# Kernel tuning notes

Hardware: AMD Instinct MI355X
Metric: run time of the kernel (lower is better)

The kernel has to match this reference:

```python
import jax, jax.numpy as jnp
import numpy as np

NUM_HEADS = 8

def setup_inputs() -> dict:
    key = jax.random.key(0)
    ks = jax.random.split(key, 6)
    B, nW, F_W, ED = 8, 64, 128, 512
    x = jax.random.normal(ks[0], (B * nW, F_W, ED), dtype=jnp.float32)
    adj_mask = jax.random.normal(ks[1], (B, NUM_HEADS, F_W, F_W), dtype=jnp.float32)
    qkv_w = jax.random.normal(ks[2], (ED, 3 * ED), dtype=jnp.float32) * (ED ** -0.5)
    qkv_b = jax.random.normal(ks[3], (3 * ED,), dtype=jnp.float32) * 0.02
    proj_w = jax.random.normal(ks[4], (ED, ED), dtype=jnp.float32) * (ED ** -0.5)
    proj_b = jax.random.normal(ks[5], (ED,), dtype=jnp.float32) * 0.02
    return {"x": x, "adj_mask": adj_mask, "qkv_w": qkv_w, "qkv_b": qkv_b,
            "proj_w": proj_w, "proj_b": proj_b, "B": B, "nW": nW}

def reference(x, adj_mask, qkv_w, qkv_b, proj_w, proj_b, B, nW):
    B_nW, F_W, ED = x.shape
    H = NUM_HEADS
    hd = ED // H
    scale = hd ** -0.5
    # qkv projection: [B_nW, F_W, 3, H, hd]
    qkv = (x @ qkv_w + qkv_b).reshape(B_nW, F_W, 3, H, hd)
    qkv = jnp.transpose(qkv, (2, 0, 3, 1, 4))  # [3, B_nW, H, F_W, hd]
    q, k, v = qkv[0], qkv[1], qkv[2]
    attn = jnp.einsum('bhqd,bhkd->bhqk', q * scale, k)  # [B_nW, H, F_W, F_W]
    # additive adjacency mask, broadcast over windows
    attn = attn.reshape(B, nW, H, F_W, F_W) + adj_mask[:, None]
    attn = attn.reshape(B_nW, H, F_W, F_W)
    attn = jax.nn.softmax(attn, axis=-1)
    out = jnp.einsum('bhqk,bhkd->bhqd', attn, v)  # [B_nW, H, F_W, hd]
    out = jnp.transpose(out, (0, 2, 1, 3)).reshape(B_nW, F_W, ED)
    return out @ proj_w + proj_b
```

## Files before the change

kernel.cpp:

```cpp
#include <hip/hip_runtime.h>

typedef __bf16 bf16_t;
typedef __bf16 bf16x8 __attribute__((ext_vector_type(8)));
typedef float f32x4 __attribute__((ext_vector_type(4)));

#define MFMA16(a, b, c) __builtin_amdgcn_mfma_f32_16x16x32_bf16(a, b, c, 0, 0, 0)

#define F_W 128
#define ED 512
#define NH 8
#define HD 64
#define B_NW 512
#define NTOK 65536

typedef const __attribute__((address_space(1))) void gvoid_t;
typedef __attribute__((address_space(3))) void lvoid_t;
__device__ __forceinline__ void gload16(const void* g, void* l) {
    __builtin_amdgcn_global_load_lds((gvoid_t*)g, (lvoid_t*)l, 16, 0, 0);
}

__device__ __forceinline__ int swz32(int row) { return ((row >> 1) & 3) << 3; }

__global__ __launch_bounds__(256) void prep_kernel(
    const float* __restrict__ qkv_w,
    const float* __restrict__ proj_w,
    bf16_t* __restrict__ qkv_wt,
    bf16_t* __restrict__ proj_wt) {
    int idx = blockIdx.x * 256 + threadIdx.x;
    if (idx < 1536 * 512) {
        int n = idx >> 9, k = idx & 511;
        qkv_wt[idx] = (bf16_t)qkv_w[k * 1536 + n];
    }
    if (idx < 512 * 512) {
        int n = idx >> 9, k = idx & 511;
        proj_wt[idx] = (bf16_t)proj_w[k * 512 + n];
    }
}

__global__ __launch_bounds__(256) void prep_x_kernel(
    const float* __restrict__ x, bf16_t* __restrict__ xbf) {
    size_t i = ((size_t)blockIdx.x * 256 + threadIdx.x) * 8;
    float4 v0 = *(const float4*)(x + i);
    float4 v1 = *(const float4*)(x + i + 4);
    bf16x8 o = {(bf16_t)v0.x, (bf16_t)v0.y, (bf16_t)v0.z, (bf16_t)v0.w,
                (bf16_t)v1.x, (bf16_t)v1.y, (bf16_t)v1.z, (bf16_t)v1.w};
    *(bf16x8*)(xbf + i) = o;
}

__global__ __launch_bounds__(256, 4) void qkv_gemm_kernel(
    const bf16_t* __restrict__ xbf,
    const bf16_t* __restrict__ qkv_wt,
    const float* __restrict__ qkv_b,
    bf16_t* qk_ws,
    bf16_t* vt_ws) {
    __shared__ __align__(16) char sm[18432];
    bf16_t* x_s = (bf16_t*)sm;
    bf16_t* w_s = (bf16_t*)(sm + 8192);
    bf16_t* tb  = (bf16_t*)sm;

    const int tid = threadIdx.x;
    const int wave = tid >> 6, lane = tid & 63;
    const int lrow = lane & 15, lgrp = lane >> 4;
    const int wm = wave >> 1, wn = wave & 1;
    const int bid = blockIdx.x;
    const int idx = bid >> 3;
    const int mt_l = idx / 12;
    const int nt = idx - mt_l * 12;
    const int mtile = (bid & 7) * 64 + mt_l;
    const size_t m0 = (size_t)mtile * 128;
    const int n0 = nt * 128;

    const int row16 = lane >> 2;
    const int scol = ((lane & 3) * 8) ^ swz32(row16);

    f32x4 acc[4][4];
#pragma unroll
    for (int mf = 0; mf < 4; ++mf)
#pragma unroll
        for (int nf = 0; nf < 4; ++nf) acc[mf][nf] = (f32x4)0.0f;

    for (int kc = 0; kc < 16; ++kc) {
        const int k0 = kc * 32;
        __syncthreads();
#pragma unroll
        for (int i = 0; i < 2; ++i) {
            int c = wave * 2 + i;
            gload16(xbf + (m0 + c * 16 + row16) * 512 + k0 + scol, x_s + c * 512);
        }
#pragma unroll
        for (int i = 0; i < 2; ++i) {
            int c = wave * 2 + i;
            gload16(qkv_wt + (size_t)(n0 + c * 16 + row16) * 512 + k0 + scol,
                    w_s + c * 512);
        }
        __syncthreads();

        bf16x8 a[4], b[4];
#pragma unroll
        for (int mf = 0; mf < 4; ++mf) {
            int row = wm * 64 + mf * 16 + lrow;
            a[mf] = *(const bf16x8*)(x_s + row * 32 + ((lgrp * 8) ^ swz32(row)));
        }
#pragma unroll
        for (int nf = 0; nf < 4; ++nf) {
            int rw = wn * 64 + nf * 16 + lrow;
            b[nf] = *(const bf16x8*)(w_s + rw * 32 + ((lgrp * 8) ^ swz32(rw)));
        }
#pragma unroll
        for (int mf = 0; mf < 4; ++mf)
#pragma unroll
            for (int nf = 0; nf < 4; ++nf)
                acc[mf][nf] = MFMA16(a[mf], b[nf], acc[mf][nf]);
    }

    if (nt < 8) {
        const float scale = (nt < 4) ? 0.125f : 1.0f;
#pragma unroll
        for (int nf = 0; nf < 4; ++nf) {
            int col = n0 + wn * 64 + nf * 16 + lrow;
            float bv = qkv_b[col];
#pragma unroll
            for (int mf = 0; mf < 4; ++mf)
#pragma unroll
                for (int j = 0; j < 4; ++j) {
                    int r = wm * 64 + mf * 16 + lgrp * 4 + j;
                    qk_ws[(m0 + r) * 1024 + col] =
                        (bf16_t)((acc[mf][nf][j] + bv) * scale);
                }
        }
    } else {
#pragma unroll
        for (int hh = 0; hh < 2; ++hh) {
            int h = (nt - 8) * 2 + hh;
            __syncthreads();
            if (wn == hh) {
#pragma unroll
                for (int nf = 0; nf < 4; ++nf) {
                    int d = nf * 16 + lrow;
                    float bv = qkv_b[n0 + hh * 64 + d];
#pragma unroll
                    for (int mf = 0; mf < 4; ++mf)
#pragma unroll
                        for (int j = 0; j < 4; ++j) {
                            int r = wm * 64 + mf * 16 + lgrp * 4 + j;
                            tb[r * 72 + d] = (bf16_t)(acc[mf][nf][j] + bv);
                        }
                }
            }
            __syncthreads();
            {
                int d = tid & 63;
                int kh = tid >> 6;
                bf16_t* outp = vt_ws + ((size_t)(mtile * 8 + h) * 64 + d) * 128 + kh * 32;
#pragma unroll
                for (int o = 0; o < 4; ++o) {
                    bf16x8 v;
#pragma unroll
                    for (int e = 0; e < 8; ++e)
                        v[e] = tb[(kh * 32 + o * 8 + e) * 72 + d];
                    *(bf16x8*)(outp + o * 8) = v;
                }
            }
        }
    }
}

__global__ __launch_bounds__(512, 4) void attn_kernel(
    bf16_t* qk_ws,
    const bf16_t* __restrict__ vt_ws,
    const float* __restrict__ adj) {
    __shared__ __align__(16) char sm[32768];
    bf16_t* k_lds  = (bf16_t*)sm;
    bf16_t* vt_lds = (bf16_t*)(sm + 16384);
    bf16_t* pbuf   = (bf16_t*)sm;

    const int tid = threadIdx.x;
    const int wave = tid >> 6, lane = tid & 63;
    const int lrow = lane & 15, lgrp = lane >> 4;
    const int bid = blockIdx.x;
    const int w = (bid & 7) * 64 + (bid >> 6);
    const int h = (bid >> 3) & 7;
    const int bidx = bid & 7;

    bf16_t* qrow = qk_ws + (size_t)w * 128 * 1024;

    {
        const int krow_l = lane >> 3;
        const int kcol_l = ((lane & 7) * 8) ^ ((krow_l & 7) << 3);
#pragma unroll
        for (int i = 0; i < 2; ++i) {
            int c = wave * 2 + i;
            gload16(qrow + (size_t)(c * 8 + krow_l) * 1024 + 512 + h * 64 + kcol_l,
                    k_lds + c * 512);
        }
    }
    {
        const bf16_t* vtb = vt_ws + (size_t)(w * 8 + h) * 64 * 128;
        const int vrow_l = lane >> 4;
#pragma unroll
        for (int i = 0; i < 2; ++i) {
            int c = wave * 2 + i;
            int d = c * 4 + vrow_l;
            int vcol = ((lane & 15) * 8) ^ ((d & 7) << 3);
            gload16(vtb + (size_t)d * 128 + vcol, vt_lds + c * 512);
        }
    }
    bf16x8 aq[2];
    {
        int row = wave * 16 + lrow;
#pragma unroll
        for (int kb = 0; kb < 2; ++kb)
            aq[kb] = *(const bf16x8*)(qrow + (size_t)row * 1024 + h * 64 + kb * 32 + lgrp * 8);
    }
    __syncthreads();

    f32x4 sacc[8];
#pragma unroll
    for (int nf = 0; nf < 8; ++nf) sacc[nf] = (f32x4)0.0f;
#pragma unroll
    for (int kb = 0; kb < 2; ++kb) {
        bf16x8 b[8];
#pragma unroll
        for (int nf = 0; nf < 8; ++nf) {
            int row = nf * 16 + lrow;
            b[nf] = *(const bf16x8*)(k_lds + row * 64 + ((kb * 32 + lgrp * 8) ^ ((row & 7) << 3)));
        }
#pragma unroll
        for (int nf = 0; nf < 8; ++nf)
            sacc[nf] = MFMA16(aq[kb], b[nf], sacc[nf]);
    }

    const float* mbase = adj + ((size_t)(bidx * NH + h)) * F_W * F_W;
#pragma unroll
    for (int j = 0; j < 4; ++j) {
        int row = wave * 16 + lgrp * 4 + j;
        const float* mrow = mbase + (size_t)row * F_W;
        float mx = -1e30f;
#pragma unroll
        for (int nf = 0; nf < 8; ++nf) {
            sacc[nf][j] += mrow[nf * 16 + lrow];
            mx = fmaxf(mx, sacc[nf][j]);
        }
#pragma unroll
        for (int d = 1; d < 16; d <<= 1) mx = fmaxf(mx, __shfl_xor(mx, d));
        float sum = 0.f;
#pragma unroll
        for (int nf = 0; nf < 8; ++nf) {
            float p = exp2f((sacc[nf][j] - mx) * 1.44269504f);
            sacc[nf][j] = p;
            sum += p;
        }
#pragma unroll
        for (int d = 1; d < 16; d <<= 1) sum += __shfl_xor(sum, d);
        float r = 1.0f / sum;
#pragma unroll
        for (int nf = 0; nf < 8; ++nf) sacc[nf][j] *= r;
    }
    __syncthreads();

    f32x4 oacc[4];
#pragma unroll
    for (int nf = 0; nf < 4; ++nf) oacc[nf] = (f32x4)0.0f;

#pragma unroll
    for (int kb = 0; kb < 4; ++kb) {
#pragma unroll
        for (int nn = 0; nn < 2; ++nn) {
            int nf = kb * 2 + nn;
            int kk = nn * 16 + lrow;
#pragma unroll
            for (int j = 0; j < 4; ++j) {
                int r = wave * 16 + lgrp * 4 + j;
                pbuf[r * 40 + kk] = (bf16_t)(sacc[nf][j]);
            }
        }
        __syncthreads();
        bf16x8 a = *(const bf16x8*)(pbuf + (wave * 16 + lrow) * 40 + lgrp * 8);
        bf16x8 b[4];
#pragma unroll
        for (int nf = 0; nf < 4; ++nf) {
            int d = nf * 16 + lrow;
            b[nf] = *(const bf16x8*)(vt_lds + d * 128 + ((kb * 32 + lgrp * 8) ^ ((d & 7) << 3)));
        }
#pragma unroll
        for (int nf = 0; nf < 4; ++nf)
            oacc[nf] = MFMA16(a, b[nf], oacc[nf]);
        __syncthreads();
    }

#pragma unroll
    for (int nf = 0; nf < 4; ++nf) {
        int ocol = h * 64 + nf * 16 + lrow;
#pragma unroll
        for (int j = 0; j < 4; ++j) {
            int r = wave * 16 + lgrp * 4 + j;
            qrow[(size_t)r * 1024 + ocol] = (bf16_t)oacc[nf][j];
        }
    }
}

__global__ __launch_bounds__(256, 4) void proj_kernel(
    const bf16_t* __restrict__ a_g,
    const bf16_t* __restrict__ bt_g,
    const float* __restrict__ bias,
    float* __restrict__ out) {
    __shared__ __align__(16) bf16_t sm_[8192];
    bf16_t* a_s = sm_;
    bf16_t* b_s = sm_ + 4096;
    const int tid = threadIdx.x;
    const int wave = tid >> 6, lane = tid & 63;
    const int lrow = lane & 15, lgrp = lane >> 4;
    const int wm = wave >> 1, wn = wave & 1;
    const int bid = blockIdx.x;
    const int mtile = (bid & 7) * 64 + (bid >> 5);
    const int ntile = (bid >> 3) & 3;
    const size_t m0 = (size_t)mtile * 128;
    const int n0 = ntile * 128;
    const int row16 = lane >> 2;
    const int scol = ((lane & 3) * 8) ^ swz32(row16);

    f32x4 acc[4][4];
#pragma unroll
    for (int mf = 0; mf < 4; ++mf)
#pragma unroll
        for (int nf = 0; nf < 4; ++nf) acc[mf][nf] = (f32x4)0.0f;

    for (int kc = 0; kc < 16; ++kc) {
        const int k0 = kc * 32;
        __syncthreads();
#pragma unroll
        for (int i = 0; i < 2; ++i) {
            int c = wave * 2 + i;
            gload16(a_g + (m0 + c * 16 + row16) * 1024 + k0 + scol, a_s + c * 512);
            gload16(bt_g + (size_t)(n0 + c * 16 + row16) * 512 + k0 + scol, b_s + c * 512);
        }
        __syncthreads();
        bf16x8 a[4], b[4];
#pragma unroll
        for (int mf = 0; mf < 4; ++mf) {
            int row = wm * 64 + mf * 16 + lrow;
            a[mf] = *(const bf16x8*)(a_s + row * 32 + ((lgrp * 8) ^ swz32(row)));
        }
#pragma unroll
        for (int nf = 0; nf < 4; ++nf) {
            int rw = wn * 64 + nf * 16 + lrow;
            b[nf] = *(const bf16x8*)(b_s + rw * 32 + ((lgrp * 8) ^ swz32(rw)));
        }
#pragma unroll
        for (int mf = 0; mf < 4; ++mf)
#pragma unroll
            for (int nf = 0; nf < 4; ++nf)
                acc[mf][nf] = MFMA16(a[mf], b[nf], acc[mf][nf]);
    }

#pragma unroll
    for (int nf = 0; nf < 4; ++nf) {
        int col = n0 + wn * 64 + nf * 16 + lrow;
        float bv = bias[col];
#pragma unroll
        for (int mf = 0; mf < 4; ++mf)
#pragma unroll
            for (int j = 0; j < 4; ++j) {
                size_t row = m0 + wm * 64 + mf * 16 + lgrp * 4 + j;
                out[row * 512 + col] = acc[mf][nf][j] + bv;
            }
    }
}

extern "C" void kernel_launch(void* const* d_in, const int* in_sizes, int n_in,
                              void* d_out, int out_size, void* d_ws, size_t ws_size,
                              hipStream_t stream) {
    const float* x      = (const float*)d_in[0];
    const float* adj    = (const float*)d_in[1];
    const float* qkv_w  = (const float*)d_in[2];
    const float* qkv_b  = (const float*)d_in[3];
    const float* proj_w = (const float*)d_in[4];
    const float* proj_b = (const float*)d_in[5];
    float* out = (float*)d_out;

    bf16_t* qk_ws   = (bf16_t*)d_ws;
    bf16_t* vt_ws   = qk_ws + (size_t)NTOK * 1024;
    bf16_t* qkv_wt  = vt_ws + (size_t)4096 * 64 * 128;
    bf16_t* proj_wt = qkv_wt + 1536 * 512;
    bf16_t* xbf = (bf16_t*)d_out;

    prep_kernel<<<3072, 256, 0, stream>>>(qkv_w, proj_w, qkv_wt, proj_wt);
    prep_x_kernel<<<NTOK * ED / 8 / 256, 256, 0, stream>>>(x, xbf);
    qkv_gemm_kernel<<<6144, 256, 0, stream>>>(xbf, qkv_wt, qkv_b, qk_ws, vt_ws);
    attn_kernel<<<4096, 512, 0, stream>>>(qk_ws, vt_ws, adj);
    proj_kernel<<<2048, 256, 0, stream>>>(qk_ws, proj_wt, proj_b, out);
}
```

Before: 317.2 us.

## Double-buffer activation tiles and load weight fragments directly from global in GEMMs

Both the QKV and projection GEMMs now double-buffer the activation tile in LDS with a 64-wide K step, prefetching the next chunk while computing the current one. This halves the number of barriers per tile. Weight fragments are read straight from global memory (L2-cached) into registers instead of being staged through LDS. The aim is to hide global-load latency and cut synchronisation, at the cost of larger LDS use (32KB) and more registers, which may reduce occupancy under launch_bounds(256,4).

```diff
diff --git a/kernel.cpp b/kernel.cpp
--- a/kernel.cpp
+++ b/kernel.cpp
@@ -53,10 +53,8 @@
     const float* __restrict__ qkv_b,
     bf16_t* qk_ws,
     bf16_t* vt_ws) {
-    __shared__ __align__(16) char sm[18432];
-    bf16_t* x_s = (bf16_t*)sm;
-    bf16_t* w_s = (bf16_t*)(sm + 8192);
-    bf16_t* tb  = (bf16_t*)sm;
+    __shared__ __align__(16) char sm[32768];
+    bf16_t* tb = (bf16_t*)sm;
 
     const int tid = threadIdx.x;
     const int wave = tid >> 6, lane = tid & 63;
@@ -73,44 +71,62 @@
     const int row16 = lane >> 2;
     const int scol = ((lane & 3) * 8) ^ swz32(row16);
 
+    const bf16_t* bbase = qkv_wt + (size_t)(n0 + wn * 64 + lrow) * 512 + lgrp * 8;
+
     f32x4 acc[4][4];
 #pragma unroll
     for (int mf = 0; mf < 4; ++mf)
 #pragma unroll
         for (int nf = 0; nf < 4; ++nf) acc[mf][nf] = (f32x4)0.0f;
 
-    for (int kc = 0; kc < 16; ++kc) {
-        const int k0 = kc * 32;
-        __syncthreads();
+#pragma unroll
+    for (int s = 0; s < 2; ++s)
 #pragma unroll
         for (int i = 0; i < 2; ++i) {
             int c = wave * 2 + i;
-            gload16(xbf + (m0 + c * 16 + row16) * 512 + k0 + scol, x_s + c * 512);
-        }
-#pragma unroll
-        for (int i = 0; i < 2; ++i) {
-            int c = wave * 2 + i;
-            gload16(qkv_wt + (size_t)(n0 + c * 16 + row16) * 512 + k0 + scol,
-                    w_s + c * 512);
+            gload16(xbf + (m0 + c * 16 + row16) * 512 + s * 32 + scol,
+                    (bf16_t*)(sm + s * 8192) + c * 512);
+        }
+    __syncthreads();
+
+#pragma unroll 2
+    for (int kc = 0; kc < 8; ++kc) {
+        char* cur = sm + (kc & 1) * 16384;
+        char* nxt = sm + ((kc & 1) ^ 1) * 16384;
+        const int k0 = kc * 64;
+        bf16x8 b[2][4];
+#pragma unroll
+        for (int kb = 0; kb < 2; ++kb)
+#pragma unroll
+            for (int nf = 0; nf < 4; ++nf)
+                b[kb][nf] = *(const bf16x8*)(bbase + (size_t)nf * 16 * 512 + k0 + kb * 32);
+        if (kc < 7) {
+            const int k1 = (kc + 1) * 64;
+#pragma unroll
+            for (int s = 0; s < 2; ++s)
+#pragma unroll
+                for (int i = 0; i < 2; ++i) {
+                    int c = wave * 2 + i;
+                    gload16(xbf + (m0 + c * 16 + row16) * 512 + k1 + s * 32 + scol,
+                            (bf16_t*)(nxt + s * 8192) + c * 512);
+                }
+        }
+#pragma unroll
+        for (int kb = 0; kb < 2; ++kb) {
+            bf16x8 a[4];
+#pragma unroll
+            for (int mf = 0; mf < 4; ++mf) {
+                int row = wm * 64 + mf * 16 + lrow;
+                a[mf] = *(const bf16x8*)((bf16_t*)(cur + kb * 8192) + row * 32 +
+                                         ((lgrp * 8) ^ swz32(row)));
+            }
+#pragma unroll
+            for (int mf = 0; mf < 4; ++mf)
+#pragma unroll
+                for (int nf = 0; nf < 4; ++nf)
+                    acc[mf][nf] = MFMA16(a[mf], b[kb][nf], acc[mf][nf]);
         }
         __syncthreads();
-
-        bf16x8 a[4], b[4];
-#pragma unroll
-        for (int mf = 0; mf < 4; ++mf) {
-            int row = wm * 64 + mf * 16 + lrow;
-            a[mf] = *(const bf16x8*)(x_s + row * 32 + ((lgrp * 8) ^ swz32(row)));
-        }
-#pragma unroll
-        for (int nf = 0; nf < 4; ++nf) {
-            int rw = wn * 64 + nf * 16 + lrow;
-            b[nf] = *(const bf16x8*)(w_s + rw * 32 + ((lgrp * 8) ^ swz32(rw)));
-        }
-#pragma unroll
-        for (int mf = 0; mf < 4; ++mf)
-#pragma unroll
-            for (int nf = 0; nf < 4; ++nf)
-                acc[mf][nf] = MFMA16(a[mf], b[nf], acc[mf][nf]);
     }
 
     if (nt < 8) {
@@ -304,9 +320,7 @@
     const bf16_t* __restrict__ bt_g,
     const float* __restrict__ bias,
     float* __restrict__ out) {
-    __shared__ __align__(16) bf16_t sm_[8192];
-    bf16_t* a_s = sm_;
-    bf16_t* b_s = sm_ + 4096;
+    __shared__ __align__(16) char sm_[32768];
     const int tid = threadIdx.x;
     const int wave = tid >> 6, lane = tid & 63;
     const int lrow = lane & 15, lgrp = lane >> 4;
@@ -318,6 +332,7 @@
     const int n0 = ntile * 128;
     const int row16 = lane >> 2;
     const int scol = ((lane & 3) * 8) ^ swz32(row16);
+    const bf16_t* bbase = bt_g + (size_t)(n0 + wn * 64 + lrow) * 512 + lgrp * 8;
 
     f32x4 acc[4][4];
 #pragma unroll
@@ -325,32 +340,54 @@
 #pragma unroll
         for (int nf = 0; nf < 4; ++nf) acc[mf][nf] = (f32x4)0.0f;
 
-    for (int kc = 0; kc < 16; ++kc) {
-        const int k0 = kc * 32;
-        __syncthreads();
+#pragma unroll
+    for (int s = 0; s < 2; ++s)
 #pragma unroll
         for (int i = 0; i < 2; ++i) {
             int c = wave * 2 + i;
-            gload16(a_g + (m0 + c * 16 + row16) * 1024 + k0 + scol, a_s + c * 512);
-            gload16(bt_g + (size_t)(n0 + c * 16 + row16) * 512 + k0 + scol, b_s + c * 512);
+            gload16(a_g + (m0 + c * 16 + row16) * 1024 + s * 32 + scol,
+                    (bf16_t*)(sm_ + s * 8192) + c * 512);
+        }
+    __syncthreads();
+
+#pragma unroll 2
+    for (int kc = 0; kc < 8; ++kc) {
+        char* cur = sm_ + (kc & 1) * 16384;
+        char* nxt = sm_ + ((kc & 1) ^ 1) * 16384;
+        const int k0 = kc * 64;
+        bf16x8 b[2][4];
+#pragma unroll
+        for (int kb = 0; kb < 2; ++kb)
+#pragma unroll
+            for (int nf = 0; nf < 4; ++nf)
+                b[kb][nf] = *(const bf16x8*)(bbase + (size_t)nf * 16 * 512 + k0 + kb * 32);
+        if (kc < 7) {
+            const int k1 = (kc + 1) * 64;
+#pragma unroll
+            for (int s = 0; s < 2; ++s)
+#pragma unroll
+                for (int i = 0; i < 2; ++i) {
+                    int c = wave * 2 + i;
+                    gload16(a_g + (m0 + c * 16 + row16) * 1024 + k1 + s * 32 + scol,
+                            (bf16_t*)(nxt + s * 8192) + c * 512);
+                }
+        }
+#pragma unroll
+        for (int kb = 0; kb < 2; ++kb) {
+            bf16x8 a[4];
+#pragma unroll
+            for (int mf = 0; mf < 4; ++mf) {
+                int row = wm * 64 + mf * 16 + lrow;
+                a[mf] = *(const bf16x8*)((bf16_t*)(cur + kb * 8192) + row * 32 +
+                                         ((lgrp * 8) ^ swz32(row)));
+            }
+#pragma unroll
+            for (int mf = 0; mf < 4; ++mf)
+#pragma unroll
+                for (int nf = 0; nf < 4; ++nf)
+                    acc[mf][nf] = MFMA16(a[mf], b[kb][nf], acc[mf][nf]);
         }
         __syncthreads();
-        bf16x8 a[4], b[4];
-#pragma unroll
-        for (int mf = 0; mf < 4; ++mf) {
-            int row = wm * 64 + mf * 16 + lrow;
-            a[mf] = *(const bf16x8*)(a_s + row * 32 + ((lgrp * 8) ^ swz32(row)));
-        }
-#pragma unroll
-        for (int nf = 0; nf < 4; ++nf) {
-            int rw = wn * 64 + nf * 16 + lrow;
-            b[nf] = *(const bf16x8*)(b_s + rw * 32 + ((lgrp * 8) ^ swz32(rw)));
-        }
-#pragma unroll
-        for (int mf = 0; mf < 4; ++mf)
-#pragma unroll
-            for (int nf = 0; nf < 4; ++nf)
-                acc[mf][nf] = MFMA16(a[mf], b[nf], acc[mf][nf]);
     }
 
 #pragma unroll
```

After: 448.4 us. 41.3% more time.

## Switch QKV and proj GEMMs to 32x32x16 MFMA with 64-wide K tiles

Applied to the files above, without the earlier changes.

Both GEMM kernels now use 32x32x16 bf16 MFMA instructions with 2x2 f32x16 accumulators per wave instead of 4x4 16x16x32 tiles. The K chunk per iteration doubles to 64, which halves the number of barrier pairs and global-to-LDS load rounds. The LDS swizzle is rewritten for 64-element rows. Shared memory per block grows to 32KB, which may limit occupancy at the requested 4 blocks per CU.

```diff
diff --git a/kernel.cpp b/kernel.cpp
--- a/kernel.cpp
+++ b/kernel.cpp
@@ -3,8 +3,10 @@
 typedef __bf16 bf16_t;
 typedef __bf16 bf16x8 __attribute__((ext_vector_type(8)));
 typedef float f32x4 __attribute__((ext_vector_type(4)));
+typedef float f32x16 __attribute__((ext_vector_type(16)));
 
 #define MFMA16(a, b, c) __builtin_amdgcn_mfma_f32_16x16x32_bf16(a, b, c, 0, 0, 0)
+#define MFMA32(a, b, c) __builtin_amdgcn_mfma_f32_32x32x16_bf16(a, b, c, 0, 0, 0)
 
 #define F_W 128
 #define ED 512
@@ -18,8 +20,6 @@
 __device__ __forceinline__ void gload16(const void* g, void* l) {
     __builtin_amdgcn_global_load_lds((gvoid_t*)g, (lvoid_t*)l, 16, 0, 0);
 }
-
-__device__ __forceinline__ int swz32(int row) { return ((row >> 1) & 3) << 3; }
 
 __global__ __launch_bounds__(256) void prep_kernel(
     const float* __restrict__ qkv_w,
@@ -53,14 +53,14 @@
     const float* __restrict__ qkv_b,
     bf16_t* qk_ws,
     bf16_t* vt_ws) {
-    __shared__ __align__(16) char sm[18432];
+    __shared__ __align__(16) char sm[32768];
     bf16_t* x_s = (bf16_t*)sm;
-    bf16_t* w_s = (bf16_t*)(sm + 8192);
+    bf16_t* w_s = (bf16_t*)(sm + 16384);
     bf16_t* tb  = (bf16_t*)sm;
 
     const int tid = threadIdx.x;
     const int wave = tid >> 6, lane = tid & 63;
-    const int lrow = lane & 15, lgrp = lane >> 4;
+    const int l31 = lane & 31, lhi = lane >> 5;
     const int wm = wave >> 1, wn = wave & 1;
     const int bid = blockIdx.x;
     const int idx = bid >> 3;
@@ -70,60 +70,65 @@
     const size_t m0 = (size_t)mtile * 128;
     const int n0 = nt * 128;
 
-    const int row16 = lane >> 2;
-    const int scol = ((lane & 3) * 8) ^ swz32(row16);
-
-    f32x4 acc[4][4];
-#pragma unroll
-    for (int mf = 0; mf < 4; ++mf)
-#pragma unroll
-        for (int nf = 0; nf < 4; ++nf) acc[mf][nf] = (f32x4)0.0f;
-
-    for (int kc = 0; kc < 16; ++kc) {
-        const int k0 = kc * 32;
-        __syncthreads();
-#pragma unroll
-        for (int i = 0; i < 2; ++i) {
-            int c = wave * 2 + i;
-            gload16(xbf + (m0 + c * 16 + row16) * 512 + k0 + scol, x_s + c * 512);
-        }
-#pragma unroll
-        for (int i = 0; i < 2; ++i) {
-            int c = wave * 2 + i;
-            gload16(qkv_wt + (size_t)(n0 + c * 16 + row16) * 512 + k0 + scol,
+    const int srow = lane >> 3;
+    const int scol = ((lane & 7) * 8) ^ ((srow & 7) << 3);
+
+    f32x16 acc[2][2];
+#pragma unroll
+    for (int mf = 0; mf < 2; ++mf)
+#pragma unroll
+        for (int nf = 0; nf < 2; ++nf) acc[mf][nf] = (f32x16)0.0f;
+
+    for (int kc = 0; kc < 8; ++kc) {
+        const int k0 = kc * 64;
+        __syncthreads();
+#pragma unroll
+        for (int i = 0; i < 4; ++i) {
+            int c = wave * 4 + i;
+            gload16(xbf + (m0 + c * 8 + srow) * 512 + k0 + scol, x_s + c * 512);
+        }
+#pragma unroll
+        for (int i = 0; i < 4; ++i) {
+            int c = wave * 4 + i;
+            gload16(qkv_wt + (size_t)(n0 + c * 8 + srow) * 512 + k0 + scol,
                     w_s + c * 512);
         }
         __syncthreads();
 
-        bf16x8 a[4], b[4];
-#pragma unroll
-        for (int mf = 0; mf < 4; ++mf) {
-            int row = wm * 64 + mf * 16 + lrow;
-            a[mf] = *(const bf16x8*)(x_s + row * 32 + ((lgrp * 8) ^ swz32(row)));
-        }
-#pragma unroll
-        for (int nf = 0; nf < 4; ++nf) {
-            int rw = wn * 64 + nf * 16 + lrow;
-            b[nf] = *(const bf16x8*)(w_s + rw * 32 + ((lgrp * 8) ^ swz32(rw)));
-        }
-#pragma unroll
-        for (int mf = 0; mf < 4; ++mf)
-#pragma unroll
-            for (int nf = 0; nf < 4; ++nf)
-                acc[mf][nf] = MFMA16(a[mf], b[nf], acc[mf][nf]);
+#pragma unroll
+        for (int ks = 0; ks < 4; ++ks) {
+            bf16x8 a[2], b[2];
+#pragma unroll
+            for (int mf = 0; mf < 2; ++mf) {
+                int row = wm * 64 + mf * 32 + l31;
+                a[mf] = *(const bf16x8*)(x_s + row * 64 +
+                                         ((ks * 16 + lhi * 8) ^ ((row & 7) << 3)));
+            }
+#pragma unroll
+            for (int nf = 0; nf < 2; ++nf) {
+                int rw = wn * 64 + nf * 32 + l31;
+                b[nf] = *(const bf16x8*)(w_s + rw * 64 +
+                                         ((ks * 16 + lhi * 8) ^ ((rw & 7) << 3)));
+            }
+#pragma unroll
+            for (int mf = 0; mf < 2; ++mf)
+#pragma unroll
+                for (int nf = 0; nf < 2; ++nf)
+                    acc[mf][nf] = MFMA32(a[mf], b[nf], acc[mf][nf]);
+        }
     }
 
     if (nt < 8) {
         const float scale = (nt < 4) ? 0.125f : 1.0f;
 #pragma unroll
-        for (int nf = 0; nf < 4; ++nf) {
-            int col = n0 + wn * 64 + nf * 16 + lrow;
+        for (int nf = 0; nf < 2; ++nf) {
+            int col = n0 + wn * 64 + nf * 32 + l31;
             float bv = qkv_b[col];
 #pragma unroll
-            for (int mf = 0; mf < 4; ++mf)
-#pragma unroll
-                for (int j = 0; j < 4; ++j) {
-                    int r = wm * 64 + mf * 16 + lgrp * 4 + j;
+            for (int mf = 0; mf < 2; ++mf)
+#pragma unroll
+                for (int j = 0; j < 16; ++j) {
+                    int r = wm * 64 + mf * 32 + (j & 3) + 8 * (j >> 2) + 4 * lhi;
                     qk_ws[(m0 + r) * 1024 + col] =
                         (bf16_t)((acc[mf][nf][j] + bv) * scale);
                 }
@@ -135,14 +140,14 @@
             __syncthreads();
             if (wn == hh) {
 #pragma unroll
-                for (int nf = 0; nf < 4; ++nf) {
-                    int d = nf * 16 + lrow;
+                for (int nf = 0; nf < 2; ++nf) {
+                    int d = nf * 32 + l31;
                     float bv = qkv_b[n0 + hh * 64 + d];
 #pragma unroll
-                    for (int mf = 0; mf < 4; ++mf)
-#pragma unroll
-                        for (int j = 0; j < 4; ++j) {
-                            int r = wm * 64 + mf * 16 + lgrp * 4 + j;
+                    for (int mf = 0; mf < 2; ++mf)
+#pragma unroll
+                        for (int j = 0; j < 16; ++j) {
+                            int r = wm * 64 + mf * 32 + (j & 3) + 8 * (j >> 2) + 4 * lhi;
                             tb[r * 72 + d] = (bf16_t)(acc[mf][nf][j] + bv);
                         }
                 }
@@ -304,64 +309,70 @@
     const bf16_t* __restrict__ bt_g,
     const float* __restrict__ bias,
     float* __restrict__ out) {
-    __shared__ __align__(16) bf16_t sm_[8192];
-    bf16_t* a_s = sm_;
-    bf16_t* b_s = sm_ + 4096;
+    __shared__ __align__(16) char sm_[32768];
+    bf16_t* a_s = (bf16_t*)sm_;
+    bf16_t* b_s = (bf16_t*)(sm_ + 16384);
     const int tid = threadIdx.x;
     const int wave = tid >> 6, lane = tid & 63;
-    const int lrow = lane & 15, lgrp = lane >> 4;
+    const int l31 = lane & 31, lhi = lane >> 5;
     const int wm = wave >> 1, wn = wave & 1;
     const int bid = blockIdx.x;
     const int mtile = (bid & 7) * 64 + (bid >> 5);
     const int ntile = (bid >> 3) & 3;
     const size_t m0 = (size_t)mtile * 128;
     const int n0 = ntile * 128;
-    const int row16 = lane >> 2;
-    const int scol = ((lane & 3) * 8) ^ swz32(row16);
-
-    f32x4 acc[4][4];
-#pragma unroll
-    for (int mf = 0; mf < 4; ++mf)
-#pragma unroll
-        for (int nf = 0; nf < 4; ++nf) acc[mf][nf] = (f32x4)0.0f;
-
-    for (int kc = 0; kc < 16; ++kc) {
-        const int k0 = kc * 32;
-        __syncthreads();
-#pragma unroll
-        for (int i = 0; i < 2; ++i) {
-            int c = wave * 2 + i;
-            gload16(a_g + (m0 + c * 16 + row16) * 1024 + k0 + scol, a_s + c * 512);
-            gload16(bt_g + (size_t)(n0 + c * 16 + row16) * 512 + k0 + scol, b_s + c * 512);
-        }
-        __syncthreads();
-        bf16x8 a[4], b[4];
-#pragma unroll
-        for (int mf = 0; mf < 4; ++mf) {
-            int row = wm * 64 + mf * 16 + lrow;
-            a[mf] = *(const bf16x8*)(a_s + row * 32 + ((lgrp * 8) ^ swz32(row)));
-        }
-#pragma unroll
-        for (int nf = 0; nf < 4; ++nf) {
-            int rw = wn * 64 + nf * 16 + lrow;
-            b[nf] = *(const bf16x8*)(b_s + rw * 32 + ((lgrp * 8) ^ swz32(rw)));
-        }
-#pragma unroll
-        for (int mf = 0; mf < 4; ++mf)
-#pragma unroll
-            for (int nf = 0; nf < 4; ++nf)
-                acc[mf][nf] = MFMA16(a[mf], b[nf], acc[mf][nf]);
-    }
-
-#pragma unroll
-    for (int nf = 0; nf < 4; ++nf) {
-        int col = n0 + wn * 64 + nf * 16 + lrow;
+    const int srow = lane >> 3;
+    const int scol = ((lane & 7) * 8) ^ ((srow & 7) << 3);
+
+    f32x16 acc[2][2];
+#pragma unroll
+    for (int mf = 0; mf < 2; ++mf)
+#pragma unroll
+        for (int nf = 0; nf < 2; ++nf) acc[mf][nf] = (f32x16)0.0f;
+
+    for (int kc = 0; kc < 8; ++kc) {
+        const int k0 = kc * 64;
+        __syncthreads();
+#pragma unroll
+        for (int i = 0; i < 4; ++i) {
+            int c = wave * 4 + i;
+            gload16(a_g + (m0 + c * 8 + srow) * 1024 + k0 + scol, a_s + c * 512);
+            gload16(bt_g + (size_t)(n0 + c * 8 + srow) * 512 + k0 + scol, b_s + c * 512);
+        }
+        __syncthreads();
+
+#pragma unroll
+        for (int ks = 0; ks < 4; ++ks) {
+            bf16x8 a[2], b[2];
+#pragma unroll
+            for (int mf = 0; mf < 2; ++mf) {
+                int row = wm * 64 + mf * 32 + l31;
+                a[mf] = *(const bf16x8*)(a_s + row * 64 +
+                                         ((ks * 16 + lhi * 8) ^ ((row & 7) << 3)));
+            }
+#pragma unroll
+            for (int nf = 0; nf < 2; ++nf) {
+                int rw = wn * 64 + nf * 32 + l31;
+                b[nf] = *(const bf16x8*)(b_s + rw * 64 +
+                                         ((ks * 16 + lhi * 8) ^ ((rw & 7) << 3)));
+            }
+#pragma unroll
+            for (int mf = 0; mf < 2; ++mf)
+#pragma unroll
+                for (int nf = 0; nf < 2; ++nf)
+                    acc[mf][nf] = MFMA32(a[mf], b[nf], acc[mf][nf]);
+        }
+    }
+
+#pragma unroll
+    for (int nf = 0; nf < 2; ++nf) {
+        int col = n0 + wn * 64 + nf * 32 + l31;
         float bv = bias[col];
 #pragma unroll
-        for (int mf = 0; mf < 4; ++mf)
-#pragma unroll
-            for (int j = 0; j < 4; ++j) {
-                size_t row = m0 + wm * 64 + mf * 16 + lgrp * 4 + j;
+        for (int mf = 0; mf < 2; ++mf)
+#pragma unroll
+            for (int j = 0; j < 16; ++j) {
+                size_t row = m0 + wm * 64 + mf * 32 + (j & 3) + 8 * (j >> 2) + 4 * lhi;
                 out[row * 512 + col] = acc[mf][nf][j] + bv;
             }
     }
```

Result: faster. 294.7 us (-7.1%).

## Widen QKV and projection GEMM tiles to 128x256 with 64-deep K stages

Applied to the files above, without the earlier changes.

Both GEMM kernels now compute 128x256 output tiles instead of 128x128, with each wave holding a 64x128 accumulator block, and they load a 64-wide K slice (two 32-wide LDS sub-buffers) per barrier pair. This halves the grid size, increases reuse of the A-tile per load, and halves the number of sync points per tile. The cost is a much larger register footprint (128 accumulator floats per lane) and 48KB LDS, with launch bounds lowered to 2 blocks per CU, so occupancy and latency hiding drop. The V-transpose epilogue is adapted to handle four heads per tile.

```diff
diff --git a/kernel.cpp b/kernel.cpp
--- a/kernel.cpp
+++ b/kernel.cpp
@@ -10,7 +10,6 @@
 #define ED 512
 #define NH 8
 #define HD 64
-#define B_NW 512
 #define NTOK 65536
 
 typedef const __attribute__((address_space(1))) void gvoid_t;
@@ -47,16 +46,14 @@
     *(bf16x8*)(xbf + i) = o;
 }
 
-__global__ __launch_bounds__(256, 4) void qkv_gemm_kernel(
+__global__ __launch_bounds__(256, 2) void qkv_gemm_kernel(
     const bf16_t* __restrict__ xbf,
     const bf16_t* __restrict__ qkv_wt,
     const float* __restrict__ qkv_b,
     bf16_t* qk_ws,
     bf16_t* vt_ws) {
-    __shared__ __align__(16) char sm[18432];
-    bf16_t* x_s = (bf16_t*)sm;
-    bf16_t* w_s = (bf16_t*)(sm + 8192);
-    bf16_t* tb  = (bf16_t*)sm;
+    __shared__ __align__(16) char sm[49152];
+    bf16_t* tb = (bf16_t*)sm;
 
     const int tid = threadIdx.x;
     const int wave = tid >> 6, lane = tid & 63;
@@ -64,60 +61,71 @@
     const int wm = wave >> 1, wn = wave & 1;
     const int bid = blockIdx.x;
     const int idx = bid >> 3;
-    const int mt_l = idx / 12;
-    const int nt = idx - mt_l * 12;
+    const int mt_l = idx / 6;
+    const int nt = idx - mt_l * 6;
     const int mtile = (bid & 7) * 64 + mt_l;
     const size_t m0 = (size_t)mtile * 128;
-    const int n0 = nt * 128;
+    const int n0 = nt * 256;
 
     const int row16 = lane >> 2;
     const int scol = ((lane & 3) * 8) ^ swz32(row16);
 
-    f32x4 acc[4][4];
+    f32x4 acc[4][8];
 #pragma unroll
     for (int mf = 0; mf < 4; ++mf)
 #pragma unroll
-        for (int nf = 0; nf < 4; ++nf) acc[mf][nf] = (f32x4)0.0f;
-
-    for (int kc = 0; kc < 16; ++kc) {
-        const int k0 = kc * 32;
-        __syncthreads();
-#pragma unroll
-        for (int i = 0; i < 2; ++i) {
-            int c = wave * 2 + i;
-            gload16(xbf + (m0 + c * 16 + row16) * 512 + k0 + scol, x_s + c * 512);
-        }
-#pragma unroll
-        for (int i = 0; i < 2; ++i) {
-            int c = wave * 2 + i;
-            gload16(qkv_wt + (size_t)(n0 + c * 16 + row16) * 512 + k0 + scol,
-                    w_s + c * 512);
-        }
-        __syncthreads();
-
-        bf16x8 a[4], b[4];
-#pragma unroll
-        for (int mf = 0; mf < 4; ++mf) {
-            int row = wm * 64 + mf * 16 + lrow;
-            a[mf] = *(const bf16x8*)(x_s + row * 32 + ((lgrp * 8) ^ swz32(row)));
-        }
-#pragma unroll
-        for (int nf = 0; nf < 4; ++nf) {
-            int rw = wn * 64 + nf * 16 + lrow;
-            b[nf] = *(const bf16x8*)(w_s + rw * 32 + ((lgrp * 8) ^ swz32(rw)));
-        }
-#pragma unroll
-        for (int mf = 0; mf < 4; ++mf)
-#pragma unroll
-            for (int nf = 0; nf < 4; ++nf)
-                acc[mf][nf] = MFMA16(a[mf], b[nf], acc[mf][nf]);
-    }
-
-    if (nt < 8) {
-        const float scale = (nt < 4) ? 0.125f : 1.0f;
-#pragma unroll
-        for (int nf = 0; nf < 4; ++nf) {
-            int col = n0 + wn * 64 + nf * 16 + lrow;
+        for (int nf = 0; nf < 8; ++nf) acc[mf][nf] = (f32x4)0.0f;
+
+    for (int kc = 0; kc < 8; ++kc) {
+        const int k0 = kc * 64;
+        __syncthreads();
+#pragma unroll
+        for (int s = 0; s < 2; ++s) {
+            bf16_t* As = (bf16_t*)(sm + s * 8192);
+            bf16_t* Bs = (bf16_t*)(sm + 16384 + s * 16384);
+#pragma unroll
+            for (int i = 0; i < 2; ++i) {
+                int c = wave * 2 + i;
+                gload16(xbf + (m0 + c * 16 + row16) * 512 + k0 + s * 32 + scol,
+                        As + c * 512);
+            }
+#pragma unroll
+            for (int i = 0; i < 4; ++i) {
+                int c = wave * 4 + i;
+                gload16(qkv_wt + (size_t)(n0 + c * 16 + row16) * 512 + k0 + s * 32 + scol,
+                        Bs + c * 512);
+            }
+        }
+        __syncthreads();
+
+#pragma unroll
+        for (int kb = 0; kb < 2; ++kb) {
+            bf16_t* As = (bf16_t*)(sm + kb * 8192);
+            bf16_t* Bs = (bf16_t*)(sm + 16384 + kb * 16384);
+            bf16x8 a[4], b[8];
+#pragma unroll
+            for (int mf = 0; mf < 4; ++mf) {
+                int row = wm * 64 + mf * 16 + lrow;
+                a[mf] = *(const bf16x8*)(As + row * 32 + ((lgrp * 8) ^ swz32(row)));
+            }
+#pragma unroll
+            for (int nf = 0; nf < 8; ++nf) {
+                int rw = wn * 128 + nf * 16 + lrow;
+                b[nf] = *(const bf16x8*)(Bs + rw * 32 + ((lgrp * 8) ^ swz32(rw)));
+            }
+#pragma unroll
+            for (int mf = 0; mf < 4; ++mf)
+#pragma unroll
+                for (int nf = 0; nf < 8; ++nf)
+                    acc[mf][nf] = MFMA16(a[mf], b[nf], acc[mf][nf]);
+        }
+    }
+
+    if (nt < 4) {
+        const float scale = (nt < 2) ? 0.125f : 1.0f;
+#pragma unroll
+        for (int nf = 0; nf < 8; ++nf) {
+            int col = n0 + wn * 128 + nf * 16 + lrow;
             float bv = qkv_b[col];
 #pragma unroll
             for (int mf = 0; mf < 4; ++mf)
@@ -130,14 +138,15 @@
         }
     } else {
 #pragma unroll
-        for (int hh = 0; hh < 2; ++hh) {
-            int h = (nt - 8) * 2 + hh;
+        for (int hh = 0; hh < 4; ++hh) {
+            int h = (nt - 4) * 4 + hh;
             __syncthreads();
-            if (wn == hh) {
-#pragma unroll
-                for (int nf = 0; nf < 4; ++nf) {
-                    int d = nf * 16 + lrow;
-                    float bv = qkv_b[n0 + hh * 64 + d];
+            if (wn == (hh >> 1)) {
+#pragma unroll
+                for (int nfl = 0; nfl < 4; ++nfl) {
+                    int nf = (hh & 1) * 4 + nfl;
+                    int d = nfl * 16 + lrow;
+                    float bv = qkv_b[1024 + (nt - 4) * 256 + hh * 64 + d];
 #pragma unroll
                     for (int mf = 0; mf < 4; ++mf)
 #pragma unroll
@@ -299,63 +308,79 @@
     }
 }
 
-__global__ __launch_bounds__(256, 4) void proj_kernel(
+__global__ __launch_bounds__(256, 2) void proj_kernel(
     const bf16_t* __restrict__ a_g,
     const bf16_t* __restrict__ bt_g,
     const float* __restrict__ bias,
     float* __restrict__ out) {
-    __shared__ __align__(16) bf16_t sm_[8192];
-    bf16_t* a_s = sm_;
-    bf16_t* b_s = sm_ + 4096;
+    __shared__ __align__(16) char sm_[49152];
     const int tid = threadIdx.x;
     const int wave = tid >> 6, lane = tid & 63;
     const int lrow = lane & 15, lgrp = lane >> 4;
     const int wm = wave >> 1, wn = wave & 1;
     const int bid = blockIdx.x;
-    const int mtile = (bid & 7) * 64 + (bid >> 5);
-    const int ntile = (bid >> 3) & 3;
+    const int idx = bid >> 3;
+    const int mtile = (bid & 7) * 64 + (idx >> 1);
+    const int ntile = idx & 1;
     const size_t m0 = (size_t)mtile * 128;
-    const int n0 = ntile * 128;
+    const int n0 = ntile * 256;
     const int row16 = lane >> 2;
     const int scol = ((lane & 3) * 8) ^ swz32(row16);
 
-    f32x4 acc[4][4];
+    f32x4 acc[4][8];
 #pragma unroll
     for (int mf = 0; mf < 4; ++mf)
 #pragma unroll
-        for (int nf = 0; nf < 4; ++nf) acc[mf][nf] = (f32x4)0.0f;
-
-    for (int kc = 0; kc < 16; ++kc) {
-        const int k0 = kc * 32;
-        __syncthreads();
-#pragma unroll
-        for (int i = 0; i < 2; ++i) {
-            int c = wave * 2 + i;
-            gload16(a_g + (m0 + c * 16 + row16) * 1024 + k0 + scol, a_s + c * 512);
-            gload16(bt_g + (size_t)(n0 + c * 16 + row16) * 512 + k0 + scol, b_s + c * 512);
-        }
-        __syncthreads();
-        bf16x8 a[4], b[4];
-#pragma unroll
-        for (int mf = 0; mf < 4; ++mf) {
-            int row = wm * 64 + mf * 16 + lrow;
-            a[mf] = *(const bf16x8*)(a_s + row * 32 + ((lgrp * 8) ^ swz32(row)));
-        }
-#pragma unroll
-        for (int nf = 0; nf < 4; ++nf) {
-            int rw = wn * 64 + nf * 16 + lrow;
-            b[nf] = *(const bf16x8*)(b_s + rw * 32 + ((lgrp * 8) ^ swz32(rw)));
-        }
-#pragma unroll
-        for (int mf = 0; mf < 4; ++mf)
-#pragma unroll
-            for (int nf = 0; nf < 4; ++nf)
-                acc[mf][nf] = MFMA16(a[mf], b[nf], acc[mf][nf]);
-    }
-
-#pragma unroll
-    for (int nf = 0; nf < 4; ++nf) {
-        int col = n0 + wn * 64 + nf * 16 + lrow;
+        for (int nf = 0; nf < 8; ++nf) acc[mf][nf] = (f32x4)0.0f;
+
+    for (int kc = 0; kc < 8; ++kc) {
+        const int k0 = kc * 64;
+        __syncthreads();
+#pragma unroll
+        for (int s = 0; s < 2; ++s) {
+            bf16_t* As = (bf16_t*)(sm_ + s * 8192);
+            bf16_t* Bs = (bf16_t*)(sm_ + 16384 + s * 16384);
+#pragma unroll
+            for (int i = 0; i < 2; ++i) {
+                int c = wave * 2 + i;
+                gload16(a_g + (m0 + c * 16 + row16) * 1024 + k0 + s * 32 + scol,
+                        As + c * 512);
+            }
+#pragma unroll
+            for (int i = 0; i < 4; ++i) {
+                int c = wave * 4 + i;
+                gload16(bt_g + (size_t)(n0 + c * 16 + row16) * 512 + k0 + s * 32 + scol,
+                        Bs + c * 512);
+            }
+        }
+        __syncthreads();
+
+#pragma unroll
+        for (int kb = 0; kb < 2; ++kb) {
+            bf16_t* As = (bf16_t*)(sm_ + kb * 8192);
+            bf16_t* Bs = (bf16_t*)(sm_ + 16384 + kb * 16384);
+            bf16x8 a[4], b[8];
+#pragma unroll
+            for (int mf = 0; mf < 4; ++mf) {
+                int row = wm * 64 + mf * 16 + lrow;
+                a[mf] = *(const bf16x8*)(As + row * 32 + ((lgrp * 8) ^ swz32(row)));
+            }
+#pragma unroll
+            for (int nf = 0; nf < 8; ++nf) {
+                int rw = wn * 128 + nf * 16 + lrow;
+                b[nf] = *(const bf16x8*)(Bs + rw * 32 + ((lgrp * 8) ^ swz32(rw)));
+            }
+#pragma unroll
+            for (int mf = 0; mf < 4; ++mf)
+#pragma unroll
+                for (int nf = 0; nf < 8; ++nf)
+                    acc[mf][nf] = MFMA16(a[mf], b[nf], acc[mf][nf]);
+        }
+    }
+
+#pragma unroll
+    for (int nf = 0; nf < 8; ++nf) {
+        int col = n0 + wn * 128 + nf * 16 + lrow;
         float bv = bias[col];
 #pragma unroll
         for (int mf = 0; mf < 4; ++mf)
@@ -386,7 +411,7 @@
 
     prep_kernel<<<3072, 256, 0, stream>>>(qkv_w, proj_w, qkv_wt, proj_wt);
     prep_x_kernel<<<NTOK * ED / 8 / 256, 256, 0, stream>>>(x, xbf);
-    qkv_gemm_kernel<<<6144, 256, 0, stream>>>(xbf, qkv_wt, qkv_b, qk_ws, vt_ws);
+    qkv_gemm_kernel<<<3072, 256, 0, stream>>>(xbf, qkv_wt, qkv_b, qk_ws, vt_ws);
     attn_kernel<<<4096, 512, 0, stream>>>(qk_ws, vt_ws, adj);
-    proj_kernel<<<2048, 256, 0, stream>>>(qk_ws, proj_wt, proj_b, out);
-}
+    proj_kernel<<<1024, 256, 0, stream>>>(qk_ws, proj_wt, proj_b, out);
+}
```

New measurement: 299.8 us. 5.5% less time.
